# Performance work log

Hardware: AMD Instinct MI355X
Metric: run time of the kernel (lower is better)

The kernel has to match this reference:

```python
import jax, jax.numpy as jnp
import numpy as np

N_NODES = 200000
N_EDGES = 640000
IN_DIM, H1, H2, OUT_DIM = 128, 64, 32, 20


def _glorot(key, shape):
    fan_in, fan_out = shape[0], shape[1]
    lim = float(np.sqrt(6.0 / (fan_in + fan_out)))
    return jax.random.uniform(key, shape, jnp.float32, -lim, lim)


def setup_inputs() -> dict:
    key = jax.random.key(0)
    ks = jax.random.split(key, 8)
    x = jax.random.normal(ks[0], (N_NODES, IN_DIM), jnp.float32)
    edge_index = jax.random.randint(ks[1], (2, N_EDGES), 0, N_NODES, jnp.int64)
    # SAGEConv params: lin_l (neighbor path, with bias), lin_r (root path, no bias)
    return {
        "x": x,
        "edge_index": edge_index,
        "Wl1": _glorot(ks[2], (IN_DIM, H1)), "bl1": jnp.zeros((H1,), jnp.float32),
        "Wr1": _glorot(ks[3], (IN_DIM, H1)),
        "Wl2": _glorot(ks[4], (H1, H2)), "bl2": jnp.zeros((H2,), jnp.float32),
        "Wr2": _glorot(ks[5], (H1, H2)),
        "Wl3": _glorot(ks[6], (H2, OUT_DIM)), "bl3": jnp.zeros((OUT_DIM,), jnp.float32),
        "Wr3": _glorot(ks[7], (H2, OUT_DIM)),
    }


def _sage_conv(x, src, dst, inv_deg, Wl, bl, Wr):
    # mean-aggregate neighbor features: scatter-add x[src] into dst, divide by in-degree
    msgs = x[src]                                            # [E, D] gather
    agg = jax.ops.segment_sum(msgs, dst, num_segments=N_NODES)  # [N, D]
    agg = agg * inv_deg[:, None]                             # mean
    return agg @ Wl + bl + x @ Wr                            # lin_l(agg) + lin_r(x)


def reference(x, edge_index, Wl1, bl1, Wr1, Wl2, bl2, Wr2, Wl3, bl3, Wr3):
    src, dst = edge_index[0], edge_index[1]
    deg = jax.ops.segment_sum(jnp.ones((src.shape[0],), x.dtype), dst,
                              num_segments=N_NODES)
    inv_deg = jnp.where(deg > 0, 1.0 / jnp.maximum(deg, 1.0), 0.0)

    h = jax.nn.relu(_sage_conv(x, src, dst, inv_deg, Wl1, bl1, Wr1))
    # dropout layers are identity in eval mode
    h = jax.nn.relu(_sage_conv(h, src, dst, inv_deg, Wl2, bl2, Wr2))
    return _sage_conv(h, src, dst, inv_deg, Wl3, bl3, Wr3)
```

## Files before the change

### kernel.cpp

```cpp
#include <hip/hip_runtime.h>
#include <hip/hip_bf16.h>


typedef __attribute__((ext_vector_type(8))) short short8;
typedef __attribute__((ext_vector_type(4))) float f32x4;

__device__ inline unsigned short f2b(float x) {
    return __bfloat16_as_ushort(__float2bfloat16(x));
}
__device__ inline float b2f(unsigned short u) {
    return __uint_as_float(((unsigned)u) << 16);
}

__device__ __forceinline__ void gload_lds16(const void* g, void* l) {
    __builtin_amdgcn_global_load_lds(
        (const __attribute__((address_space(1))) void*)g,
        (__attribute__((address_space(3))) void*)l, 16, 0, 0);
}


__global__ void hist_kernel(const int* __restrict__ dst, int* __restrict__ deg, int E) {
    int i = blockIdx.x * blockDim.x + threadIdx.x;
    if (i < E) atomicAdd(&deg[dst[i]], 1);
}

__global__ void scan_reduce(const int* __restrict__ deg, int* __restrict__ bsum, int n) {
    __shared__ int s[256];
    int i = blockIdx.x * 256 + threadIdx.x;
    s[threadIdx.x] = (i < n) ? deg[i] : 0;
    __syncthreads();
    for (int off = 128; off > 0; off >>= 1) {
        if (threadIdx.x < off) s[threadIdx.x] += s[threadIdx.x + off];
        __syncthreads();
    }
    if (threadIdx.x == 0) bsum[blockIdx.x] = s[0];
}

__global__ void scan_top(int* __restrict__ bsum, int nb) {
    __shared__ int s[1024];
    int t = threadIdx.x;
    int v = (t < nb) ? bsum[t] : 0;
    s[t] = v;
    __syncthreads();
    for (int off = 1; off < 1024; off <<= 1) {
        int add = (t >= off) ? s[t - off] : 0;
        __syncthreads();
        s[t] += add;
        __syncthreads();
    }
    if (t < nb) bsum[t] = s[t] - v;
}

__global__ void scan_final(const int* __restrict__ deg, const int* __restrict__ bsum,
                           int* __restrict__ rowptr, int* __restrict__ cursor,
                           int n, int E) {
    __shared__ int s[256];
    int t = threadIdx.x;
    int i = blockIdx.x * 256 + t;
    int v = (i < n) ? deg[i] : 0;
    s[t] = v;
    __syncthreads();
    for (int off = 1; off < 256; off <<= 1) {
        int add = (t >= off) ? s[t - off] : 0;
        __syncthreads();
        s[t] += add;
        __syncthreads();
    }
    int excl = s[t] - v + bsum[blockIdx.x];
    if (i < n) {
        rowptr[i] = excl;
        cursor[i] = excl;
    }
    if (i == 0) rowptr[n] = E;
}

__global__ void fill_kernel(const int* __restrict__ src, const int* __restrict__ dst,
                            int* __restrict__ cursor, int* __restrict__ csr, int E) {
    int e = blockIdx.x * blockDim.x + threadIdx.x;
    if (e < E) {
        int pos = atomicAdd(&cursor[dst[e]], 1);
        csr[pos] = src[e];
    }
}


__launch_bounds__(256, 2)
__global__ void proj1_mfma(const float* __restrict__ x,
                           const float* __restrict__ Wl,
                           const float* __restrict__ Wr,
                           const float* __restrict__ bl,
                           unsigned short* __restrict__ pv,
                           unsigned short* __restrict__ rv,
                           int n) {
    constexpr int S = 4;
    constexpr int TWB = 4;
    constexpr int NCH = TWB * S * 64;

    __shared__ __attribute__((aligned(16))) unsigned short sW[NCH * 8];
    __shared__ __attribute__((aligned(16))) float sX[2][64 * 128];

    const int b = (int)blockIdx.x;
    const int ch = (b >> 3) & 1;
    const int blk = (b & 7) | ((b >> 4) << 3);
    const int nblk = (int)gridDim.x >> 1;

    const int tid = threadIdx.x;
    for (int chunk = tid; chunk < NCH; chunk += 256) {
        const int lane_c = chunk & 63;
        const int rest = chunk >> 6;
        const int s = rest % S;
        const int t = rest / S;
        const int c = (ch * TWB + t) * 16 + (lane_c & 15);
        const int k0 = s * 32 + (lane_c >> 4) * 8;
        short8 pack;
#pragma unroll
        for (int j = 0; j < 8; ++j) {
            const int k = k0 + j;
            float w = (c < 64) ? Wl[k * 64 + c] : Wr[k * 64 + (c - 64)];
            pack[j] = (short)f2b(w);
        }
        *reinterpret_cast<short8*>(&sW[(size_t)chunk * 8]) = pack;
    }

    const int wave = tid >> 6, lane = tid & 63;
    const int rg = wave;
    const int q = lane >> 4, ln = lane & 15;

    int colg[4];
    float bias[4];
#pragma unroll
    for (int t = 0; t < 4; ++t) {
        colg[t] = ch * 64 + t * 16 + ln;
        bias[t] = (colg[t] >= 64) ? bl[colg[t] - 64] : 0.0f;
    }

    auto stage = [&](int d, int nb) {
#pragma unroll
        for (int i = 0; i < 8; ++i) {
            const int cbase = wave * 512 + i * 64;
            const int ci = cbase + lane;
            const int rl = ci >> 5;
            const int cc = ci & 31;
            int row = nb + rl;
            if (row >= n) row = n - 1;
            const float* g = x + (size_t)row * 128 + (size_t)((cc ^ (rl & 7)) << 2);
            char* l = (char*)&sX[d][0] + (size_t)cbase * 16;
            gload_lds16(g, l);
        }
    };

    auto compute = [&](int d, int nb) {
        const int rowb = nb + rg * 16;
        const int rl = rg * 16 + ln;
        const int swz = rl & 7;
        const float* xbase = &sX[d][(size_t)rl * 128];
        f32x4 acc[4];
#pragma unroll
        for (int t = 0; t < 4; ++t) acc[t] = (f32x4){0.f, 0.f, 0.f, 0.f};
#pragma unroll
        for (int s = 0; s < S; ++s) {
            const int c0 = s * 8 + q * 2;
            float4 v0 = *reinterpret_cast<const float4*>(xbase + ((c0 ^ swz) << 2));
            float4 v1 = *reinterpret_cast<const float4*>(xbase + (((c0 + 1) ^ swz) << 2));
            short8 a;
            a[0] = (short)f2b(v0.x); a[1] = (short)f2b(v0.y);
            a[2] = (short)f2b(v0.z); a[3] = (short)f2b(v0.w);
            a[4] = (short)f2b(v1.x); a[5] = (short)f2b(v1.y);
            a[6] = (short)f2b(v1.z); a[7] = (short)f2b(v1.w);
#pragma unroll
            for (int t = 0; t < 4; ++t) {
                short8 bf = *reinterpret_cast<const short8*>(
                    &sW[((size_t)(t * S + s)) * 512 + (size_t)lane * 8]);
                acc[t] = __builtin_amdgcn_mfma_f32_16x16x32_bf16(a, bf, acc[t], 0, 0, 0);
            }
        }
#pragma unroll
        for (int t = 0; t < 4; ++t) {
            const int c = colg[t];
#pragma unroll
            for (int rr = 0; rr < 4; ++rr) {
                const int row = rowb + q * 4 + rr;
                if (row < n) {
                    if (c < 64)
                        pv[(size_t)row * 64 + c] = f2b(acc[t][rr]);
                    else
                        rv[(size_t)row * 64 + (c - 64)] = f2b(acc[t][rr] + bias[t]);
                }
            }
        }
    };

    constexpr int npi = 64;
    const int stride = nblk * npi;
    int nb = blk * npi;
    if (nb >= n) return;
    stage(0, nb);
    __syncthreads();
    while (true) {
        const int nb1 = nb + stride;
        if (nb1 < n) stage(1, nb1);
        compute(0, nb);
        __syncthreads();
        if (nb1 >= n) break;
        const int nb2 = nb1 + stride;
        if (nb2 < n) stage(0, nb2);
        compute(1, nb1);
        __syncthreads();
        nb = nb2;
        if (nb >= n) break;
    }
}


template <int DIN, int DP, int DR, int DT2, bool RELU, bool OUT_BF16>
__launch_bounds__(256, 4)
__global__ void proj_lds(const unsigned short* __restrict__ xv,
                         const float* __restrict__ Wl,
                         const float* __restrict__ Wr,
                         const float* __restrict__ bl,
                         void* __restrict__ pv,
                         void* __restrict__ rv,
                         int n) {
    constexpr int S = DIN / 32;
    constexpr int TILES = DT2 / 16;
    constexpr int CR = DIN / 8;
    constexpr int NCH = TILES * S * 64;

    __shared__ __attribute__((aligned(16))) unsigned short sW[NCH * 8];
    __shared__ __attribute__((aligned(16))) unsigned short sX[2][64 * DIN];

    const int blk = (int)blockIdx.x;
    const int nblk = (int)gridDim.x;
    const int tid = threadIdx.x;

    for (int chunk = tid; chunk < NCH; chunk += 256) {
        const int lane_c = chunk & 63;
        const int rest = chunk >> 6;
        const int s = rest % S;
        const int t = rest / S;
        const int c = t * 16 + (lane_c & 15);
        const int k0 = s * 32 + (lane_c >> 4) * 8;
        short8 pack;
#pragma unroll
        for (int j = 0; j < 8; ++j) {
            float w = 0.f;
            const int k = k0 + j;
            if (c < DP) w = Wl[k * DP + c];
            else if (c < DP + DR) w = Wr[k * DR + (c - DP)];
            pack[j] = (short)f2b(w);
        }
        *reinterpret_cast<short8*>(&sW[(size_t)chunk * 8]) = pack;
    }

    const int wave = tid >> 6, lane = tid & 63;
    const int rg = wave;
    const int q = lane >> 4, ln = lane & 15;

    int colg[TILES];
    float bias[TILES];
#pragma unroll
    for (int t = 0; t < TILES; ++t) {
        colg[t] = t * 16 + ln;
        bias[t] = (colg[t] >= DP && colg[t] < DP + DR) ? bl[colg[t] - DP] : 0.0f;
    }

    auto stage = [&](int d, int nb) {
#pragma unroll
        for (int i = 0; i < CR / 4; ++i) {
            const int cbase = wave * (16 * CR) + i * 64;
            const int ci = cbase + lane;
            const int rl = ci / CR;
            const int cc = ci & (CR - 1);
            int row = nb + rl;
            if (row >= n) row = n - 1;
            const unsigned short* g =
                xv + (size_t)row * DIN + (size_t)((cc ^ (rl & (CR - 1))) << 3);
            char* l = (char*)&sX[d][0] + (size_t)cbase * 16;
            gload_lds16(g, l);
        }
    };

    auto compute = [&](int d, int nb) {
        const int rl = rg * 16 + ln;
        const int swz = rl & (CR - 1);
        const unsigned short* rowb = &sX[d][(size_t)rl * DIN];
        f32x4 acc[TILES];
#pragma unroll
        for (int t = 0; t < TILES; ++t) acc[t] = (f32x4){0.f, 0.f, 0.f, 0.f};
#pragma unroll
        for (int s = 0; s < S; ++s) {
            const int c0 = s * 4 + q;
            short8 a = *reinterpret_cast<const short8*>(rowb + (size_t)((c0 ^ swz) << 3));
            if (RELU) {
#pragma unroll
                for (int j = 0; j < 8; ++j)
                    a[j] = ((short)a[j] < 0) ? (short)0 : a[j];
            }
#pragma unroll
            for (int t = 0; t < TILES; ++t) {
                short8 bf = *reinterpret_cast<const short8*>(
                    &sW[((size_t)(t * S + s)) * 512 + (size_t)lane * 8]);
                acc[t] = __builtin_amdgcn_mfma_f32_16x16x32_bf16(a, bf, acc[t], 0, 0, 0);
            }
        }
        const int rowbase = nb + rg * 16 + q * 4;
#pragma unroll
        for (int t = 0; t < TILES; ++t) {
            const int c = colg[t];
#pragma unroll
            for (int rr = 0; rr < 4; ++rr) {
                const int row = rowbase + rr;
                if (row < n) {
                    if (c < DP) {
                        if constexpr (OUT_BF16)
                            ((unsigned short*)pv)[(size_t)row * DP + c] = f2b(acc[t][rr]);
                        else
                            ((float*)pv)[(size_t)row * DP + c] = acc[t][rr];
                    } else if (c < DP + DR) {
                        const float v = acc[t][rr] + bias[t];
                        if constexpr (OUT_BF16)
                            ((unsigned short*)rv)[(size_t)row * DR + (c - DP)] = f2b(v);
                        else
                            ((float*)rv)[(size_t)row * DR + (c - DP)] = v;
                    }
                }
            }
        }
    };

    constexpr int npi = 64;
    const int stride = nblk * npi;
    int nb = blk * npi;
    if (nb >= n) return;
    stage(0, nb);
    __syncthreads();
    while (true) {
        const int nb1 = nb + stride;
        if (nb1 < n) stage(1, nb1);
        compute(0, nb);
        __syncthreads();
        if (nb1 >= n) break;
        const int nb2 = nb1 + stride;
        if (nb2 < n) stage(0, nb2);
        compute(1, nb1);
        __syncthreads();
        nb = nb2;
        if (nb >= n) break;
    }
}


template <int D, int L>
__global__ void agg_bf16(const int* __restrict__ rowptr,
                         const int* __restrict__ csr,
                         const unsigned short* __restrict__ p,
                         unsigned short* __restrict__ out,
                         int n) {
    constexpr int RQ = D / 8;
    long long gid = (long long)blockIdx.x * blockDim.x + threadIdx.x;
    int d = (int)(gid / L);
    int l = (int)(gid % L);
    if (d >= n) return;
    int beg = rowptr[d], end = rowptr[d + 1];
    int deg = end - beg;
    if (deg <= 0) return;

    const short8* pr = reinterpret_cast<const short8*>(p);
    float s[8];
#pragma unroll
    for (int j = 0; j < 8; ++j) s[j] = 0.0f;

    int i = beg;
    for (; i + 4 <= end; i += 4) {
        int e0 = csr[i], e1 = csr[i + 1], e2 = csr[i + 2], e3 = csr[i + 3];
        short8 a = pr[(size_t)e0 * RQ + l];
        short8 b = pr[(size_t)e1 * RQ + l];
        short8 c = pr[(size_t)e2 * RQ + l];
        short8 e = pr[(size_t)e3 * RQ + l];
#pragma unroll
        for (int j = 0; j < 8; ++j)
            s[j] += (b2f((unsigned short)a[j]) + b2f((unsigned short)b[j])) +
                    (b2f((unsigned short)c[j]) + b2f((unsigned short)e[j]));
    }
    for (; i < end; ++i) {
        short8 a = pr[(size_t)csr[i] * RQ + l];
#pragma unroll
        for (int j = 0; j < 8; ++j) s[j] += b2f((unsigned short)a[j]);
    }

    const float inv = 1.0f / (float)deg;
    short8* o = reinterpret_cast<short8*>(out) + (size_t)d * RQ + l;
    short8 cur = *o;
#pragma unroll
    for (int j = 0; j < 8; ++j) {
        float v = b2f((unsigned short)cur[j]) + s[j] * inv;
        cur[j] = (short)f2b(v);
    }
    *o = cur;
}

template <int D, int L>
__global__ void agg_f32(const int* __restrict__ rowptr,
                        const int* __restrict__ csr,
                        const float* __restrict__ p,
                        float* __restrict__ out,
                        int n) {
    constexpr int RQ = D / 4;
    static_assert(L == RQ, "agg_f32: one float4 per lane");
    long long gid = (long long)blockIdx.x * blockDim.x + threadIdx.x;
    int d = (int)(gid / L);
    int l = (int)(gid % L);
    if (d >= n) return;
    int beg = rowptr[d], end = rowptr[d + 1];
    int deg = end - beg;
    if (deg <= 0) return;

    const float4* pr = reinterpret_cast<const float4*>(p);
    float sx = 0.f, sy = 0.f, sz = 0.f, sw = 0.f;
    int i = beg;
    for (; i + 4 <= end; i += 4) {
        int s0 = csr[i], s1 = csr[i + 1], s2 = csr[i + 2], s3 = csr[i + 3];
        float4 a = pr[(size_t)s0 * RQ + l];
        float4 b = pr[(size_t)s1 * RQ + l];
        float4 c = pr[(size_t)s2 * RQ + l];
        float4 e = pr[(size_t)s3 * RQ + l];
        sx += (a.x + b.x) + (c.x + e.x);
        sy += (a.y + b.y) + (c.y + e.y);
        sz += (a.z + b.z) + (c.z + e.z);
        sw += (a.w + b.w) + (c.w + e.w);
    }
    for (; i < end; ++i) {
        float4 a = pr[(size_t)csr[i] * RQ + l];
        sx += a.x; sy += a.y; sz += a.z; sw += a.w;
    }
    const float inv = 1.0f / (float)deg;
    float4* o = reinterpret_cast<float4*>(out) + (size_t)d * RQ + l;
    float4 cur = *o;
    cur.x += sx * inv; cur.y += sy * inv;
    cur.z += sz * inv; cur.w += sw * inv;
    *o = cur;
}


extern "C" void kernel_launch(void* const* d_in, const int* in_sizes, int n_in,
                              void* d_out, int out_size, void* d_ws, size_t ws_size,
                              hipStream_t stream) {
    const float* x   = (const float*)d_in[0];
    const int*   ei  = (const int*)d_in[1];
    const float* Wl1 = (const float*)d_in[2];
    const float* bl1 = (const float*)d_in[3];
    const float* Wr1 = (const float*)d_in[4];
    const float* Wl2 = (const float*)d_in[5];
    const float* bl2 = (const float*)d_in[6];
    const float* Wr2 = (const float*)d_in[7];
    const float* Wl3 = (const float*)d_in[8];
    const float* bl3 = (const float*)d_in[9];
    const float* Wr3 = (const float*)d_in[10];
    float* out = (float*)d_out;

    const int N = in_sizes[0] / 128;
    const int E = in_sizes[1] / 2;
    const int* src  = ei;
    const int* dstp = ei + E;

    unsigned short* A1 = (unsigned short*)d_ws;
    unsigned short* Bb = A1 + (size_t)N * 64;
    unsigned short* A2 = Bb + (size_t)N * 64;
    unsigned short* Cb = A2 + (size_t)N * 32;
    float* A3 = (float*)(Cb + (size_t)N * 32);
    int* rowptr = (int*)(A3 + (size_t)N * 20);
    int* csr    = rowptr + (N + 1);

    int* degi   = (int*)A3;
    int* cursor = degi + N;
    int* bsum   = cursor + N;

    const int NB = (N + 255) / 256;

    hipMemsetAsync(degi, 0, (size_t)N * sizeof(int), stream);
    hist_kernel<<<(E + 255) / 256, 256, 0, stream>>>(dstp, degi, E);
    scan_reduce<<<NB, 256, 0, stream>>>(degi, bsum, N);
    scan_top<<<1, 1024, 0, stream>>>(bsum, NB);
    scan_final<<<NB, 256, 0, stream>>>(degi, bsum, rowptr, cursor, N, E);
    fill_kernel<<<(E + 255) / 256, 256, 0, stream>>>(src, dstp, cursor, csr, E);

    proj1_mfma<<<512, 256, 0, stream>>>(x, Wl1, Wr1, bl1, A1, Bb, N);
    agg_bf16<64, 8><<<(int)(((long long)N * 8 + 255) / 256), 256, 0, stream>>>(
        rowptr, csr, A1, Bb, N);

    proj_lds<64, 32, 32, 64, true, true><<<1024, 256, 0, stream>>>(
        Bb, Wl2, Wr2, bl2, A2, Cb, N);
    agg_bf16<32, 4><<<(int)(((long long)N * 4 + 255) / 256), 256, 0, stream>>>(
        rowptr, csr, A2, Cb, N);

    proj_lds<32, 20, 20, 48, true, false><<<1024, 256, 0, stream>>>(
        Cb, Wl3, Wr3, bl3, A3, out, N);
    agg_f32<20, 5><<<(int)(((long long)N * 5 + 255) / 256), 256, 0, stream>>>(
        rowptr, csr, A3, out, N);
}
```

Baseline: 333.2 us.

## Fuse CSR construction into one cooperative kernel with grid syncs

Replaces the memset and the five CSR-build kernels (histogram, three scan stages, fill) with a single cooperative kernel. Phases are separated by grid.sync(), and the top-level scan runs in chunks inside block 0. The aim is to remove per-kernel launch gaps and drain/refill costs between stages. In exchange it adds five grid-wide barriers, and the cooperative launch of 782 blocks must fit co-resident on the device.

```diff
diff --git a/kernel.cpp b/kernel.cpp
--- a/kernel.cpp
+++ b/kernel.cpp
@@ -1,5 +1,8 @@
 #include <hip/hip_runtime.h>
 #include <hip/hip_bf16.h>
+#include <hip/hip_cooperative_groups.h>
+
+namespace cg = cooperative_groups;
 
 
 typedef __attribute__((ext_vector_type(8))) short short8;
@@ -19,65 +22,80 @@
 }
 
 
-__global__ void hist_kernel(const int* __restrict__ dst, int* __restrict__ deg, int E) {
-    int i = blockIdx.x * blockDim.x + threadIdx.x;
-    if (i < E) atomicAdd(&deg[dst[i]], 1);
-}
-
-__global__ void scan_reduce(const int* __restrict__ deg, int* __restrict__ bsum, int n) {
+__launch_bounds__(256, 4)
+__global__ void csr_build(const int* __restrict__ src, const int* __restrict__ dst,
+                          int* __restrict__ degi, int* __restrict__ bsum,
+                          int* __restrict__ rowptr, int* __restrict__ cursor,
+                          int* __restrict__ csr, int n, int E, int nb) {
+    cg::grid_group grid = cg::this_grid();
     __shared__ int s[256];
-    int i = blockIdx.x * 256 + threadIdx.x;
-    s[threadIdx.x] = (i < n) ? deg[i] : 0;
-    __syncthreads();
-    for (int off = 128; off > 0; off >>= 1) {
-        if (threadIdx.x < off) s[threadIdx.x] += s[threadIdx.x + off];
-        __syncthreads();
-    }
-    if (threadIdx.x == 0) bsum[blockIdx.x] = s[0];
-}
-
-__global__ void scan_top(int* __restrict__ bsum, int nb) {
-    __shared__ int s[1024];
-    int t = threadIdx.x;
-    int v = (t < nb) ? bsum[t] : 0;
-    s[t] = v;
-    __syncthreads();
-    for (int off = 1; off < 1024; off <<= 1) {
-        int add = (t >= off) ? s[t - off] : 0;
-        __syncthreads();
-        s[t] += add;
-        __syncthreads();
-    }
-    if (t < nb) bsum[t] = s[t] - v;
-}
-
-__global__ void scan_final(const int* __restrict__ deg, const int* __restrict__ bsum,
-                           int* __restrict__ rowptr, int* __restrict__ cursor,
-                           int n, int E) {
-    __shared__ int s[256];
-    int t = threadIdx.x;
-    int i = blockIdx.x * 256 + t;
-    int v = (i < n) ? deg[i] : 0;
-    s[t] = v;
-    __syncthreads();
-    for (int off = 1; off < 256; off <<= 1) {
-        int add = (t >= off) ? s[t - off] : 0;
-        __syncthreads();
-        s[t] += add;
-        __syncthreads();
-    }
-    int excl = s[t] - v + bsum[blockIdx.x];
-    if (i < n) {
-        rowptr[i] = excl;
-        cursor[i] = excl;
-    }
-    if (i == 0) rowptr[n] = E;
-}
-
-__global__ void fill_kernel(const int* __restrict__ src, const int* __restrict__ dst,
-                            int* __restrict__ cursor, int* __restrict__ csr, int E) {
-    int e = blockIdx.x * blockDim.x + threadIdx.x;
-    if (e < E) {
+    __shared__ int carry;
+
+    const int tid = threadIdx.x;
+    const int gtid = (int)blockIdx.x * 256 + tid;
+    const int gsz = (int)gridDim.x * 256;
+
+    for (int i = gtid; i < n; i += gsz) degi[i] = 0;
+    grid.sync();
+
+    for (int e = gtid; e < E; e += gsz) atomicAdd(&degi[dst[e]], 1);
+    grid.sync();
+
+    {
+        int v = (gtid < n) ? degi[gtid] : 0;
+        s[tid] = v;
+        __syncthreads();
+        for (int off = 128; off > 0; off >>= 1) {
+            if (tid < off) s[tid] += s[tid + off];
+            __syncthreads();
+        }
+        if (tid == 0) bsum[blockIdx.x] = s[0];
+    }
+    grid.sync();
+
+    if (blockIdx.x == 0) {
+        if (tid == 0) carry = 0;
+        __syncthreads();
+        for (int base = 0; base < nb; base += 256) {
+            const int idx = base + tid;
+            const int val = (idx < nb) ? bsum[idx] : 0;
+            s[tid] = val;
+            __syncthreads();
+            for (int off = 1; off < 256; off <<= 1) {
+                int add = (tid >= off) ? s[tid - off] : 0;
+                __syncthreads();
+                s[tid] += add;
+                __syncthreads();
+            }
+            const int incl = s[tid] + carry;
+            if (idx < nb) bsum[idx] = incl - val;
+            __syncthreads();
+            if (tid == 255) carry = incl;
+            __syncthreads();
+        }
+    }
+    grid.sync();
+
+    {
+        int v = (gtid < n) ? degi[gtid] : 0;
+        s[tid] = v;
+        __syncthreads();
+        for (int off = 1; off < 256; off <<= 1) {
+            int add = (tid >= off) ? s[tid - off] : 0;
+            __syncthreads();
+            s[tid] += add;
+            __syncthreads();
+        }
+        const int excl = s[tid] - v + bsum[blockIdx.x];
+        if (gtid < n) {
+            rowptr[gtid] = excl;
+            cursor[gtid] = excl;
+        }
+        if (gtid == 0) rowptr[n] = E;
+    }
+    grid.sync();
+
+    for (int e = gtid; e < E; e += gsz) {
         int pos = atomicAdd(&cursor[dst[e]], 1);
         csr[pos] = src[e];
     }
@@ -477,12 +495,14 @@
 
     const int NB = (N + 255) / 256;
 
-    hipMemsetAsync(degi, 0, (size_t)N * sizeof(int), stream);
-    hist_kernel<<<(E + 255) / 256, 256, 0, stream>>>(dstp, degi, E);
-    scan_reduce<<<NB, 256, 0, stream>>>(degi, bsum, N);
-    scan_top<<<1, 1024, 0, stream>>>(bsum, NB);
-    scan_final<<<NB, 256, 0, stream>>>(degi, bsum, rowptr, cursor, N, E);
-    fill_kernel<<<(E + 255) / 256, 256, 0, stream>>>(src, dstp, cursor, csr, E);
+    {
+        int n_ = N, e_ = E, nb_ = NB;
+        void* args[] = {(void*)&src, (void*)&dstp, (void*)&degi, (void*)&bsum,
+                        (void*)&rowptr, (void*)&cursor, (void*)&csr,
+                        (void*)&n_, (void*)&e_, (void*)&nb_};
+        hipLaunchCooperativeKernel(reinterpret_cast<void*>(csr_build),
+                                   dim3(NB), dim3(256), args, 0, stream);
+    }
 
     proj1_mfma<<<512, 256, 0, stream>>>(x, Wl1, Wr1, bl1, A1, Bb, N);
     agg_bf16<64, 8><<<(int)(((long long)N * 8 + 255) / 256), 256, 0, stream>>>(
```

Result: slower. 736.7 us (+121.1%).

## Fuse degree histogram into layer-1 projection and replace three-pass scan with atomic allocation

Applied to the files above, without the earlier changes.

The in-degree histogram now runs inside the first projection kernel as a grid-stride atomic loop, which removes a separate launch. The three scan kernels are collapsed into a single scan_alloc kernel: each block scans its slice locally and claims a base offset through an atomic counter, a decoupled allocation rather than a global prefix sum. The CSR segments are therefore no longer in node order, so the aggregation kernels read degree from the deg array instead of rowptr[d+1]. This cuts launches and the single-block scan_top bottleneck, at the cost of non-contiguous segment ordering, possibly worse locality, and extra atomics contending with the projection work.

```diff
diff --git a/kernel.cpp b/kernel.cpp
--- a/kernel.cpp
+++ b/kernel.cpp
@@ -19,59 +19,29 @@
 }
 
 
-__global__ void hist_kernel(const int* __restrict__ dst, int* __restrict__ deg, int E) {
-    int i = blockIdx.x * blockDim.x + threadIdx.x;
-    if (i < E) atomicAdd(&deg[dst[i]], 1);
-}
-
-__global__ void scan_reduce(const int* __restrict__ deg, int* __restrict__ bsum, int n) {
+__global__ void scan_alloc(const int* __restrict__ deg, int* __restrict__ counter,
+                           int* __restrict__ rowptr, int* __restrict__ cursor,
+                           int n) {
     __shared__ int s[256];
-    int i = blockIdx.x * 256 + threadIdx.x;
-    s[threadIdx.x] = (i < n) ? deg[i] : 0;
-    __syncthreads();
-    for (int off = 128; off > 0; off >>= 1) {
-        if (threadIdx.x < off) s[threadIdx.x] += s[threadIdx.x + off];
-        __syncthreads();
-    }
-    if (threadIdx.x == 0) bsum[blockIdx.x] = s[0];
-}
-
-__global__ void scan_top(int* __restrict__ bsum, int nb) {
-    __shared__ int s[1024];
-    int t = threadIdx.x;
-    int v = (t < nb) ? bsum[t] : 0;
-    s[t] = v;
-    __syncthreads();
-    for (int off = 1; off < 1024; off <<= 1) {
-        int add = (t >= off) ? s[t - off] : 0;
-        __syncthreads();
-        s[t] += add;
-        __syncthreads();
-    }
-    if (t < nb) bsum[t] = s[t] - v;
-}
-
-__global__ void scan_final(const int* __restrict__ deg, const int* __restrict__ bsum,
-                           int* __restrict__ rowptr, int* __restrict__ cursor,
-                           int n, int E) {
-    __shared__ int s[256];
-    int t = threadIdx.x;
-    int i = blockIdx.x * 256 + t;
-    int v = (i < n) ? deg[i] : 0;
-    s[t] = v;
+    __shared__ int base;
+    const int tid = threadIdx.x;
+    const int i = (int)blockIdx.x * 256 + tid;
+    const int v = (i < n) ? deg[i] : 0;
+    s[tid] = v;
     __syncthreads();
     for (int off = 1; off < 256; off <<= 1) {
-        int add = (t >= off) ? s[t - off] : 0;
-        __syncthreads();
-        s[t] += add;
-        __syncthreads();
-    }
-    int excl = s[t] - v + bsum[blockIdx.x];
+        int add = (tid >= off) ? s[tid - off] : 0;
+        __syncthreads();
+        s[tid] += add;
+        __syncthreads();
+    }
+    if (tid == 255) base = atomicAdd(counter, s[255]);
+    __syncthreads();
+    const int excl = s[tid] - v + base;
     if (i < n) {
         rowptr[i] = excl;
         cursor[i] = excl;
     }
-    if (i == 0) rowptr[n] = E;
 }
 
 __global__ void fill_kernel(const int* __restrict__ src, const int* __restrict__ dst,
@@ -91,7 +61,9 @@
                            const float* __restrict__ bl,
                            unsigned short* __restrict__ pv,
                            unsigned short* __restrict__ rv,
-                           int n) {
+                           const int* __restrict__ dst,
+                           int* __restrict__ deg,
+                           int n, int E) {
     constexpr int S = 4;
     constexpr int TWB = 4;
     constexpr int NCH = TWB * S * 64;
@@ -105,6 +77,13 @@
     const int nblk = (int)gridDim.x >> 1;
 
     const int tid = threadIdx.x;
+
+    {
+        const int gsz = (int)gridDim.x * 256;
+        for (int e = b * 256 + tid; e < E; e += gsz)
+            atomicAdd(&deg[dst[e]], 1);
+    }
+
     for (int chunk = tid; chunk < NCH; chunk += 256) {
         const int lane_c = chunk & 63;
         const int rest = chunk >> 6;
@@ -251,6 +230,7 @@
         }
         *reinterpret_cast<short8*>(&sW[(size_t)chunk * 8]) = pack;
     }
+    __syncthreads();
 
     const int wave = tid >> 6, lane = tid & 63;
     const int rg = wave;
@@ -352,6 +332,7 @@
 
 template <int D, int L>
 __global__ void agg_bf16(const int* __restrict__ rowptr,
+                         const int* __restrict__ degp,
                          const int* __restrict__ csr,
                          const unsigned short* __restrict__ p,
                          unsigned short* __restrict__ out,
@@ -361,9 +342,9 @@
     int d = (int)(gid / L);
     int l = (int)(gid % L);
     if (d >= n) return;
-    int beg = rowptr[d], end = rowptr[d + 1];
-    int deg = end - beg;
+    int deg = degp[d];
     if (deg <= 0) return;
+    int beg = rowptr[d], end = beg + deg;
 
     const short8* pr = reinterpret_cast<const short8*>(p);
     float s[8];
@@ -401,6 +382,7 @@
 
 template <int D, int L>
 __global__ void agg_f32(const int* __restrict__ rowptr,
+                        const int* __restrict__ degp,
                         const int* __restrict__ csr,
                         const float* __restrict__ p,
                         float* __restrict__ out,
@@ -411,9 +393,9 @@
     int d = (int)(gid / L);
     int l = (int)(gid % L);
     if (d >= n) return;
-    int beg = rowptr[d], end = rowptr[d + 1];
-    int deg = end - beg;
+    int deg = degp[d];
     if (deg <= 0) return;
+    int beg = rowptr[d], end = beg + deg;
 
     const float4* pr = reinterpret_cast<const float4*>(p);
     float sx = 0.f, sy = 0.f, sz = 0.f, sw = 0.f;
@@ -469,32 +451,31 @@
     unsigned short* Cb = A2 + (size_t)N * 32;
     float* A3 = (float*)(Cb + (size_t)N * 32);
     int* rowptr = (int*)(A3 + (size_t)N * 20);
-    int* csr    = rowptr + (N + 1);
-
-    int* degi   = (int*)A3;
-    int* cursor = degi + N;
-    int* bsum   = cursor + N;
+    int* csr     = rowptr + (N + 1);
+    int* deg     = csr + E;
+    int* counter = deg + N;
+
+    int* cursor = (int*)A3;
 
     const int NB = (N + 255) / 256;
 
-    hipMemsetAsync(degi, 0, (size_t)N * sizeof(int), stream);
-    hist_kernel<<<(E + 255) / 256, 256, 0, stream>>>(dstp, degi, E);
-    scan_reduce<<<NB, 256, 0, stream>>>(degi, bsum, N);
-    scan_top<<<1, 1024, 0, stream>>>(bsum, NB);
-    scan_final<<<NB, 256, 0, stream>>>(degi, bsum, rowptr, cursor, N, E);
+    hipMemsetAsync(deg, 0, (size_t)(N + 1) * sizeof(int), stream);
+
+    proj1_mfma<<<512, 256, 0, stream>>>(x, Wl1, Wr1, bl1, A1, Bb, dstp, deg, N, E);
+
+    scan_alloc<<<NB, 256, 0, stream>>>(deg, counter, rowptr, cursor, N);
     fill_kernel<<<(E + 255) / 256, 256, 0, stream>>>(src, dstp, cursor, csr, E);
 
-    proj1_mfma<<<512, 256, 0, stream>>>(x, Wl1, Wr1, bl1, A1, Bb, N);
     agg_bf16<64, 8><<<(int)(((long long)N * 8 + 255) / 256), 256, 0, stream>>>(
-        rowptr, csr, A1, Bb, N);
+        rowptr, deg, csr, A1, Bb, N);
 
     proj_lds<64, 32, 32, 64, true, true><<<1024, 256, 0, stream>>>(
         Bb, Wl2, Wr2, bl2, A2, Cb, N);
     agg_bf16<32, 4><<<(int)(((long long)N * 4 + 255) / 256), 256, 0, stream>>>(
-        rowptr, csr, A2, Cb, N);
+        rowptr, deg, csr, A2, Cb, N);
 
     proj_lds<32, 20, 20, 48, true, false><<<1024, 256, 0, stream>>>(
         Cb, Wl3, Wr3, bl3, A3, out, N);
     agg_f32<20, 5><<<(int)(((long long)N * 5 + 255) / 256), 256, 0, stream>>>(
-        rowptr, csr, A3, out, N);
-}
+        rowptr, deg, csr, A3, out, N);
+}
```

Measured after the change: 334.3 us. About the same (+0.3%).
